# Kernel tuning notes

Hardware: AMD Instinct MI355X
Metric: run time of the kernel (lower is better)

The kernel has to match this reference:

```python
import jax, jax.numpy as jnp
import numpy as np

B, N_OBJ, OBJ_D = 256, 36, 2048
ATT_D, EMB_D, DEC_D, VOCAB, T = 1024, 1024, 1024, 10000, 20


def setup_inputs() -> dict:
    key = jax.random.key(0)
    ks = jax.random.split(key, 16)
    s = lambda *d: 1.0 / np.sqrt(d[-1])
    inp = {
        'encoder_out': jax.random.normal(ks[0], (B, EMB_D), jnp.float32),
        'objects': jax.random.normal(ks[1], (B, N_OBJ, OBJ_D), jnp.float32),
        'encoded_captions': jax.random.randint(ks[2], (B, T), 0, VOCAB),
        'caption_lengths': jax.random.randint(ks[3], (B, 1), 1, T + 1),
        'emb_table': jax.random.normal(ks[4], (VOCAB, EMB_D), jnp.float32) * 0.02,
        'W_enc_att': jax.random.normal(ks[5], (ATT_D, OBJ_D), jnp.float32) * s(OBJ_D),
        'b_enc_att': jnp.zeros((ATT_D,), jnp.float32),
        'W_dec_att': jax.random.normal(ks[6], (ATT_D, DEC_D), jnp.float32) * s(DEC_D),
        'b_dec_att': jnp.zeros((ATT_D,), jnp.float32),
        'w_full_att': jax.random.normal(ks[7], (1, ATT_D), jnp.float32) * s(ATT_D),
        'b_full_att': jnp.zeros((1,), jnp.float32),
        'W_fbeta': jax.random.normal(ks[8], (OBJ_D, DEC_D), jnp.float32) * s(DEC_D),
        'b_fbeta': jnp.zeros((OBJ_D,), jnp.float32),
        'W_ih': jax.random.normal(ks[9], (4 * DEC_D, EMB_D + OBJ_D), jnp.float32) * s(EMB_D + OBJ_D),
        'W_hh': jax.random.normal(ks[10], (4 * DEC_D, DEC_D), jnp.float32) * s(DEC_D),
        'b_ih': jnp.zeros((4 * DEC_D,), jnp.float32),
        'b_hh': jnp.zeros((4 * DEC_D,), jnp.float32),
        'W_fc': jax.random.normal(ks[11], (VOCAB, DEC_D), jnp.float32) * s(DEC_D),
        'b_fc': jnp.zeros((VOCAB,), jnp.float32),
    }
    return inp


def reference(encoder_out, objects, encoded_captions, caption_lengths,
              emb_table, W_enc_att, b_enc_att, W_dec_att, b_dec_att,
              w_full_att, b_full_att, W_fbeta, b_fbeta,
              W_ih, W_hh, b_ih, b_hh, W_fc, b_fc):
    lengths = caption_lengths[:, 0]
    sort_ind = jnp.argsort(-lengths)  # descending
    lengths = lengths[sort_ind]
    encoder_out = encoder_out[sort_ind]
    objects = objects[sort_ind]
    encoded_captions = encoded_captions[sort_ind]

    embeddings = emb_table[encoded_captions]  # (B, T, E)
    # step t input: encoder_out at t=0, embeddings[:, t-1] afterwards
    step_x = jnp.concatenate([encoder_out[:, None, :], embeddings[:, : T - 1, :]], axis=1)  # (B,T,E)

    att1 = jnp.einsum('bno,ao->bna', objects, W_enc_att) + b_enc_att  # (B,N,A), h-independent

    def step(carry, xs):
        h, c = carry
        x_t, t = xs  # (B,E), scalar
        active = (t < lengths)[:, None]  # (B,1) -- batch_size_t masking (lengths sorted desc)
        att2 = h @ W_dec_att.T + b_dec_att  # (B,A)
        e = (jax.nn.relu(att1 + att2[:, None, :]) @ w_full_att[0] + b_full_att[0])  # (B,N)
        alpha = jax.nn.softmax(e, axis=1)
        awe = jnp.einsum('bn,bno->bo', alpha, objects)  # (B,O)
        gate = jax.nn.sigmoid(h @ W_fbeta.T + b_fbeta)
        awe = gate * awe
        gates = jnp.concatenate([x_t, awe], axis=-1) @ W_ih.T + b_ih + h @ W_hh.T + b_hh
        i, f, g, o = jnp.split(gates, 4, axis=-1)  # torch LSTMCell order
        c_new = jax.nn.sigmoid(f) * c + jax.nn.sigmoid(i) * jnp.tanh(g)
        h_new = jax.nn.sigmoid(o) * jnp.tanh(c_new)
        h = jnp.where(active, h_new, h)
        c = jnp.where(active, c_new, c)
        preds = h_new @ W_fc.T + b_fc  # dropout in eval mode = identity
        preds = jnp.where(active, preds, 0.0)
        alpha = jnp.where(active, alpha, 0.0)
        return (h, c), (preds, alpha)

    h0 = jnp.zeros((B, DEC_D), objects.dtype)
    c0 = jnp.zeros((B, DEC_D), objects.dtype)
    xs = (jnp.swapaxes(step_x, 0, 1), jnp.arange(T))
    _, (preds, alphas) = jax.lax.scan(step, (h0, c0), xs)
    predictions = jnp.swapaxes(preds, 0, 1)  # (B,T,V)
    alphas = jnp.swapaxes(alphas, 0, 1)      # (B,T,N)
    return predictions, encoded_captions, lengths, alphas, sort_ind
```

## Files before the change

### kernel.cpp

```cpp
#include <hip/hip_runtime.h>
#include <hip/hip_bf16.h>
#include <cstdint>
#include <cstddef>

#define BB 256
#define TT 20
#define NOBJ 36
#define OBJD 2048
#define ATTD 1024
#define DECD 1024
#define VOCAB 10000
#define NBIG  17168
#define NBIGP 17280
#define NSPLIT 7168

typedef unsigned short u16;
typedef __attribute__((ext_vector_type(8))) short short8v;
typedef __attribute__((ext_vector_type(4))) float float4v;

__device__ inline u16 f2bf(float f) {
    __hip_bfloat16 h = __float2bfloat16(f);
    return *reinterpret_cast<u16*>(&h);
}
__device__ inline float bu(u16 u) {
    union { unsigned int i; float f; } x;
    x.i = ((unsigned int)u) << 16;
    return x.f;
}
__device__ inline float sigf(float x) { return 1.f / (1.f + expf(-x)); }

__device__ inline void gload16(const u16* g, u16* l) {
    __builtin_amdgcn_global_load_lds(
        (const __attribute__((address_space(1))) unsigned int*)g,
        (__attribute__((address_space(3))) unsigned int*)l, 16, 0, 0);
}

__global__ __launch_bounds__(256) void sort_kernel(
    const int* __restrict__ lens, int* __restrict__ sidx, int* __restrict__ slen,
    int* __restrict__ cnt, float* __restrict__ out_len, float* __restrict__ out_sind)
{
    __shared__ int L[BB];
    __shared__ int SL[BB];
    const int i = threadIdx.x;
    const int li = lens[i];
    L[i] = li;
    __syncthreads();
    int r = 0;
    for (int j = 0; j < BB; ++j) {
        const int lj = L[j];
        if (lj > li || (lj == li && j < i)) r++;
    }
    sidx[r] = i;
    slen[r] = li;
    SL[r] = li;
    out_sind[r] = (float)i;
    out_len[r]  = (float)li;
    __syncthreads();
    if (i < TT) {
        int cc = 0;
        for (int b = 0; b < BB; ++b) cc += (SL[b] > i);
        cnt[i] = cc;
    }
}

__global__ __launch_bounds__(256) void meta_kernel(
    const int* __restrict__ caps, const int* __restrict__ sidx,
    float* __restrict__ out_caps)
{
    const int idx = blockIdx.x * 256 + threadIdx.x;
    const int p = idx / TT, t = idx % TT;
    out_caps[idx] = (float)caps[sidx[p] * TT + t];
}

__global__ __launch_bounds__(256) void gather_objs(
    const float* __restrict__ objs, const int* __restrict__ sidx,
    u16* __restrict__ objsb)
{
    const int row = blockIdx.x;
    const int b = row / NOBJ, n = row - b * NOBJ;
    const float* src = objs + ((size_t)sidx[b] * NOBJ + n) * OBJD;
    u16* dst = objsb + (size_t)row * OBJD;
    const int tid = threadIdx.x;
    #pragma unroll
    for (int j = 0; j < 2; ++j) {
        float4 v = ((const float4*)src)[tid + 256 * j];
        ushort4 s;
        s.x = f2bf(v.x); s.y = f2bf(v.y); s.z = f2bf(v.z); s.w = f2bf(v.w);
        ((ushort4*)dst)[tid + 256 * j] = s;
    }
}

__global__ __launch_bounds__(256) void convWbig(
    const float* __restrict__ Wda, const float* __restrict__ bda,
    const float* __restrict__ Wfb, const float* __restrict__ bfb,
    const float* __restrict__ Whh,
    const float* __restrict__ Wfc, const float* __restrict__ bfc,
    u16* __restrict__ Wb, float* __restrict__ bcat)
{
    const int n = blockIdx.x;
    const int tid = threadIdx.x;
    const float* src = nullptr;
    float bb = 0.f;
    if (n < 1024)        { src = Wda + (size_t)n * 1024;            bb = bda[n]; }
    else if (n < 3072)   { src = Wfb + (size_t)(n - 1024) * 1024;   bb = bfb[n - 1024]; }
    else if (n < 7168)   { src = Whh + (size_t)(n - 3072) * 1024;   bb = 0.f; }
    else if (n < NBIG)   { src = Wfc + (size_t)(n - 7168) * 1024;   bb = bfc[n - 7168]; }
    u16* dst = Wb + (size_t)n * 1024;
    ushort4 s;
    if (src) {
        float4 v = ((const float4*)src)[tid];
        s.x = f2bf(v.x); s.y = f2bf(v.y); s.z = f2bf(v.z); s.w = f2bf(v.w);
    } else { s.x = s.y = s.z = s.w = 0; }
    ((ushort4*)dst)[tid] = s;
    if (tid == 0) bcat[n] = bb;
}

__global__ __launch_bounds__(256) void convWih(
    const float* __restrict__ Wih, const float* __restrict__ bih,
    const float* __restrict__ bhh, u16* __restrict__ Wb, float* __restrict__ bsum)
{
    const int n = blockIdx.x;
    const int tid = threadIdx.x;
    const float* src = Wih + (size_t)n * 3072;
    u16* dst = Wb + (size_t)n * 3072;
    #pragma unroll
    for (int j = 0; j < 3; ++j) {
        float4 v = ((const float4*)src)[tid + 256 * j];
        ushort4 s;
        s.x = f2bf(v.x); s.y = f2bf(v.y); s.z = f2bf(v.z); s.w = f2bf(v.w);
        ((ushort4*)dst)[tid + 256 * j] = s;
    }
    if (tid == 0) bsum[n] = bih[n] + bhh[n];
}

__global__ __launch_bounds__(256) void convWea(
    const float* __restrict__ Wea, u16* __restrict__ Wb)
{
    const int n = blockIdx.x;
    const int tid = threadIdx.x;
    const float* src = Wea + (size_t)n * OBJD;
    u16* dst = Wb + (size_t)n * OBJD;
    #pragma unroll
    for (int j = 0; j < 2; ++j) {
        float4 v = ((const float4*)src)[tid + 256 * j];
        ushort4 s;
        s.x = f2bf(v.x); s.y = f2bf(v.y); s.z = f2bf(v.z); s.w = f2bf(v.w);
        ((ushort4*)dst)[tid + 256 * j] = s;
    }
}

__global__ __launch_bounds__(256) void embed_kernel(
    const float* __restrict__ enc, const int* __restrict__ caps,
    const float* __restrict__ emb, const int* __restrict__ sidx,
    u16* __restrict__ Xb)
{
    const int blk = blockIdx.x;
    const int t = blk >> 8;
    const int b = blk & 255;
    const int sb = sidx[b];
    const float* src = (t == 0) ? (enc + (size_t)sb * DECD)
                                : (emb + (size_t)caps[sb * TT + (t - 1)] * DECD);
    const int tid = threadIdx.x;
    float4 v = ((const float4*)src)[tid];
    ushort4 s;
    s.x = f2bf(v.x); s.y = f2bf(v.y); s.z = f2bf(v.z); s.w = f2bf(v.w);
    ((ushort4*)(Xb + (size_t)blk * DECD))[tid] = s;
}

__global__ __launch_bounds__(256) void zero_hc(float* __restrict__ h, float* __restrict__ c)
{
    const int idx = blockIdx.x * 256 + threadIdx.x;
    if (idx < BB * DECD) h[idx] = 0.f;
    else                 c[idx - BB * DECD] = 0.f;
}

__global__ __launch_bounds__(256) void hcat0_kernel(
    const float* __restrict__ bcat, float* __restrict__ Hcat)
{
    const int col4 = blockIdx.x * 256 + threadIdx.x;
    const int m = blockIdx.y;
    ((float4*)(Hcat + (size_t)m * 7168))[col4] = ((const float4*)bcat)[col4];
}

__global__ __launch_bounds__(256) void gemm128(
    const u16* __restrict__ A, int lda,
    const u16* __restrict__ B, int ldb,
    const float* __restrict__ bias,
    float* __restrict__ Cf, u16* __restrict__ Cb, int ldc,
    int Nreal, int kzlen, size_t zCstride,
    int nsplit, float* __restrict__ C2, int ldc2, const int* __restrict__ cntp)
{
    __shared__ u16 As[128 * 32];
    __shared__ u16 Bs[128 * 32];
    const int tid = threadIdx.x;
    const int lane = tid & 63;
    const int w = tid >> 6;
    const int wr = w >> 1, wc = w & 1;
    const int m0 = blockIdx.y * 128;
    const int n0 = blockIdx.x * 128;
    const int kbase = blockIdx.z * kzlen;
    A += kbase;
    B += kbase;
    if (Cf) Cf += (size_t)blockIdx.z * zCstride;

    const int act = cntp ? *cntp : (1 << 30);
    float4v acc[4][4];
    #pragma unroll
    for (int i = 0; i < 4; ++i)
        #pragma unroll
        for (int j = 0; j < 4; ++j) acc[i][j] = (float4v){0.f, 0.f, 0.f, 0.f};

    if (m0 < act) {
        const int r0 = (w * 2 + 0) * 16 + (lane >> 2);
        const int r1 = (w * 2 + 1) * 16 + (lane >> 2);
        const int s0 = (lane & 3) ^ ((r0 >> 1) & 3);
        const int s1 = (lane & 3) ^ ((r1 >> 1) & 3);
        const u16* gA0 = A + (size_t)(m0 + r0) * lda + s0 * 8;
        const u16* gA1 = A + (size_t)(m0 + r1) * lda + s1 * 8;
        const u16* gB0 = B + (size_t)(n0 + r0) * ldb + s0 * 8;
        const u16* gB1 = B + (size_t)(n0 + r1) * ldb + s1 * 8;
        u16* lA0 = &As[(w * 2 + 0) * 16 * 32];
        u16* lA1 = &As[(w * 2 + 1) * 16 * 32];
        u16* lB0 = &Bs[(w * 2 + 0) * 16 * 32];
        u16* lB1 = &Bs[(w * 2 + 1) * 16 * 32];

        int ia[4], ib[4];
        #pragma unroll
        for (int mi = 0; mi < 4; ++mi) {
            const int r = wr * 64 + mi * 16 + (lane & 15);
            ia[mi] = r * 32 + (((lane >> 4) ^ ((r >> 1) & 3)) << 3);
        }
        #pragma unroll
        for (int nj = 0; nj < 4; ++nj) {
            const int r = wc * 64 + nj * 16 + (lane & 15);
            ib[nj] = r * 32 + (((lane >> 4) ^ ((r >> 1) & 3)) << 3);
        }

        const int nk = kzlen >> 5;
        for (int it = 0; it < nk; ++it) {
            gload16(gA0, lA0);
            gload16(gA1, lA1);
            gload16(gB0, lB0);
            gload16(gB1, lB1);
            gA0 += 32; gA1 += 32; gB0 += 32; gB1 += 32;
            __syncthreads();
            short8v av[4], bv[4];
            #pragma unroll
            for (int mi = 0; mi < 4; ++mi) av[mi] = *(const short8v*)&As[ia[mi]];
            #pragma unroll
            for (int nj = 0; nj < 4; ++nj) bv[nj] = *(const short8v*)&Bs[ib[nj]];
            #pragma unroll
            for (int mi = 0; mi < 4; ++mi)
                #pragma unroll
                for (int nj = 0; nj < 4; ++nj)
                    acc[mi][nj] = __builtin_amdgcn_mfma_f32_16x16x32_bf16(
                        av[mi], bv[nj], acc[mi][nj], 0, 0, 0);
            __syncthreads();
        }
    }

    #pragma unroll
    for (int mi = 0; mi < 4; ++mi) {
        const int mbase = m0 + wr * 64 + mi * 16 + ((lane >> 4) << 2);
        #pragma unroll
        for (int nj = 0; nj < 4; ++nj) {
            const int n = n0 + wc * 64 + nj * 16 + (lane & 15);
            if (n >= Nreal) continue;
            const float bval = bias ? bias[n] : 0.f;
            #pragma unroll
            for (int r = 0; r < 4; ++r) {
                const int m = mbase + r;
                const float v = acc[mi][nj][r] + bval;
                if (n < nsplit) {
                    if (Cb) Cb[(size_t)m * ldc + n] = f2bf(v);
                    else    Cf[(size_t)m * ldc + n] = v;
                } else {
                    C2[(size_t)m * ldc2 + (n - nsplit)] = (m < act) ? v : 0.f;
                }
            }
        }
    }
}

__global__ __launch_bounds__(256) void attn_kernel(
    const u16* __restrict__ att1b, const float* __restrict__ Hcat,
    const u16* __restrict__ objsb,
    const float* __restrict__ wfa, const float* __restrict__ bfa,
    const int* __restrict__ slen, int t,
    float* __restrict__ out_alph, u16* __restrict__ aweb)
{
    const int b = blockIdx.x, z = blockIdx.y, tid = threadIdx.x;
    const bool active = t < slen[b];
    if (!active) {
        if (z == 0 && tid < NOBJ)
            out_alph[((size_t)b * TT + t) * NOBJ + tid] = 0.f;
        return;
    }
    __shared__ float wred[4][40];
    __shared__ float es[40];
    __shared__ float alph[40];
    const int lane = tid & 63, w = tid >> 6;
    const float* hrow = Hcat + (size_t)b * 7168;
    const float4 h4 = ((const float4*)hrow)[tid];
    const float4 w4 = ((const float4*)wfa)[tid];
    const u16* a1base = att1b + (size_t)b * NOBJ * ATTD;

    float ep[NOBJ];
    #pragma unroll
    for (int n = 0; n < NOBJ; ++n) {
        ushort4 a4 = ((const ushort4*)(a1base + (size_t)n * ATTD))[tid];
        const float v0 = fmaxf(bu(a4.x) + h4.x, 0.f);
        const float v1 = fmaxf(bu(a4.y) + h4.y, 0.f);
        const float v2 = fmaxf(bu(a4.z) + h4.z, 0.f);
        const float v3 = fmaxf(bu(a4.w) + h4.w, 0.f);
        ep[n] = v0 * w4.x + v1 * w4.y + v2 * w4.z + v3 * w4.w;
    }
    #pragma unroll
    for (int n = 0; n < NOBJ; ++n) {
        float p = ep[n];
        #pragma unroll
        for (int off = 32; off > 0; off >>= 1) p += __shfl_down(p, off, 64);
        if (lane == 0) wred[w][n] = p;
    }
    __syncthreads();
    if (tid < NOBJ)
        es[tid] = wred[0][tid] + wred[1][tid] + wred[2][tid] + wred[3][tid] + bfa[0];
    __syncthreads();
    if (tid == 0) {
        float m = es[0];
        for (int n = 1; n < NOBJ; ++n) m = fmaxf(m, es[n]);
        float s = 0.f;
        for (int n = 0; n < NOBJ; ++n) { const float e = expf(es[n] - m); alph[n] = e; s += e; }
        const float inv = 1.f / s;
        for (int n = 0; n < NOBJ; ++n) alph[n] *= inv;
    }
    __syncthreads();
    if (z == 0 && tid < NOBJ)
        out_alph[((size_t)b * TT + t) * NOBJ + tid] = alph[tid];

    float acc[4] = {0.f, 0.f, 0.f, 0.f};
    const u16* ob = objsb + (size_t)b * NOBJ * OBJD + z * 1024 + tid * 4;
    #pragma unroll 4
    for (int n = 0; n < NOBJ; ++n) {
        const ushort4 ov = *(const ushort4*)(ob + (size_t)n * OBJD);
        const float al = alph[n];
        acc[0] = fmaf(al, bu(ov.x), acc[0]);
        acc[1] = fmaf(al, bu(ov.y), acc[1]);
        acc[2] = fmaf(al, bu(ov.z), acc[2]);
        acc[3] = fmaf(al, bu(ov.w), acc[3]);
    }
    const float4 g0 = *(const float4*)(hrow + 1024 + z * 1024 + tid * 4);
    ushort4 st;
    st.x = f2bf(acc[0] * sigf(g0.x));
    st.y = f2bf(acc[1] * sigf(g0.y));
    st.z = f2bf(acc[2] * sigf(g0.z));
    st.w = f2bf(acc[3] * sigf(g0.w));
    *(ushort4*)&aweb[(size_t)b * 2048 + z * 1024 + tid * 4] = st;
}

__global__ __launch_bounds__(256) void lstm_kernel(
    const float* __restrict__ G2p, const u16* __restrict__ Gxb,
    const float* __restrict__ Hcat,
    float* __restrict__ h, float* __restrict__ c, u16* __restrict__ hb,
    const int* __restrict__ slen, int t)
{
    const int idx = blockIdx.x * 256 + threadIdx.x;
    const int b = idx >> 8, d4 = idx & 255;
    if (t >= slen[b]) return;
    const float4* pw = (const float4*)(Hcat + (size_t)b * 7168 + 3072);
    const u16* gx = Gxb + ((size_t)(t * BB + b)) * 4096;

    float4 g[4];
    #pragma unroll
    for (int q = 0; q < 4; ++q) {
        const ushort4 xv = ((const ushort4*)(gx + q * 1024))[d4];
        float4 s;
        s.x = bu(xv.x); s.y = bu(xv.y); s.z = bu(xv.z); s.w = bu(xv.w);
        const float4 hv = pw[q * 256 + d4];
        s.x += hv.x; s.y += hv.y; s.z += hv.z; s.w += hv.w;
        #pragma unroll
        for (int p = 0; p < 4; ++p) {
            const float4 pv = ((const float4*)G2p)[(size_t)p * (BB * 1024) + b * 1024 + q * 256 + d4];
            s.x += pv.x; s.y += pv.y; s.z += pv.z; s.w += pv.w;
        }
        g[q] = s;
    }
    float4* hp = (float4*)(h + (size_t)b * 1024);
    float4* cp = (float4*)(c + (size_t)b * 1024);
    const float4 cold = cp[d4];
    float4 cn, hn;
    {
        const float si = sigf(g[0].x), sf = sigf(g[1].x), so = sigf(g[3].x);
        cn.x = sf * cold.x + si * tanhf(g[2].x); hn.x = so * tanhf(cn.x);
    }
    {
        const float si = sigf(g[0].y), sf = sigf(g[1].y), so = sigf(g[3].y);
        cn.y = sf * cold.y + si * tanhf(g[2].y); hn.y = so * tanhf(cn.y);
    }
    {
        const float si = sigf(g[0].z), sf = sigf(g[1].z), so = sigf(g[3].z);
        cn.z = sf * cold.z + si * tanhf(g[2].z); hn.z = so * tanhf(cn.z);
    }
    {
        const float si = sigf(g[0].w), sf = sigf(g[1].w), so = sigf(g[3].w);
        cn.w = sf * cold.w + si * tanhf(g[2].w); hn.w = so * tanhf(cn.w);
    }
    hp[d4] = hn;
    cp[d4] = cn;
    ushort4 s;
    s.x = f2bf(hn.x); s.y = f2bf(hn.y); s.z = f2bf(hn.z); s.w = f2bf(hn.w);
    ((ushort4*)(hb + (size_t)b * 1024))[d4] = s;
}

extern "C" void kernel_launch(void* const* d_in, const int* in_sizes, int n_in,
                              void* d_out, int out_size, void* d_ws, size_t ws_size,
                              hipStream_t stream)
{
    const float* enc  = (const float*)d_in[0];
    const float* objs = (const float*)d_in[1];
    const int*   caps = (const int*)d_in[2];
    const int*   clen = (const int*)d_in[3];
    const float* emb  = (const float*)d_in[4];
    const float* Wea  = (const float*)d_in[5];
    const float* bea  = (const float*)d_in[6];
    const float* Wda  = (const float*)d_in[7];
    const float* bda  = (const float*)d_in[8];
    const float* wfa  = (const float*)d_in[9];
    const float* bfa  = (const float*)d_in[10];
    const float* Wfb  = (const float*)d_in[11];
    const float* bfb  = (const float*)d_in[12];
    const float* Wih  = (const float*)d_in[13];
    const float* Whh  = (const float*)d_in[14];
    const float* bih  = (const float*)d_in[15];
    const float* bhh  = (const float*)d_in[16];
    const float* Wfc  = (const float*)d_in[17];
    const float* bfc  = (const float*)d_in[18];

    float* outP     = (float*)d_out;
    float* out_caps = outP + (size_t)BB * TT * VOCAB;
    float* out_len  = out_caps + BB * TT;
    float* out_alph = out_len + BB;
    float* out_sind = out_alph + (size_t)BB * TT * NOBJ;

    char* wp = (char*)d_ws;
    auto alloc = [&](size_t bytes) -> void* {
        void* r = (void*)wp;
        wp += (bytes + 255) & ~(size_t)255;
        return r;
    };
    int*   sidx  = (int*)alloc(BB * 4);
    int*   slen  = (int*)alloc(BB * 4);
    int*   cnt   = (int*)alloc(32 * 4);
    u16*   objsb = (u16*)alloc((size_t)BB * NOBJ * OBJD * 2);
    u16*   Wbigb = (u16*)alloc((size_t)NBIGP * 1024 * 2);
    float* bcat  = (float*)alloc(NBIGP * 4);
    u16*   Wihb  = (u16*)alloc((size_t)4096 * 3072 * 2);
    float* bsum  = (float*)alloc(4096 * 4);
    u16*   Weab  = (u16*)alloc((size_t)1024 * OBJD * 2);
    u16*   att1b = (u16*)alloc((size_t)BB * NOBJ * ATTD * 2);
    u16*   Xb    = (u16*)alloc((size_t)TT * BB * DECD * 2);
    u16*   Gxb   = (u16*)alloc((size_t)TT * BB * 4096 * 2);
    float* Hcat  = (float*)alloc((size_t)BB * 7168 * 4);
    u16*   aweb  = (u16*)alloc((size_t)BB * 2048 * 2);
    float* G2p   = (float*)alloc((size_t)4 * BB * 4096 * 4);
    float* h     = (float*)alloc((size_t)BB * DECD * 4);
    float* c     = (float*)alloc((size_t)BB * DECD * 4);
    u16*   hb    = (u16*)alloc((size_t)BB * DECD * 2);
    (void)ws_size; (void)in_sizes; (void)n_in; (void)out_size;

    sort_kernel<<<1, 256, 0, stream>>>(clen, sidx, slen, cnt, out_len, out_sind);
    meta_kernel<<<20, 256, 0, stream>>>(caps, sidx, out_caps);
    gather_objs<<<BB * NOBJ, 256, 0, stream>>>(objs, sidx, objsb);
    convWbig<<<NBIGP, 256, 0, stream>>>(Wda, bda, Wfb, bfb, Whh, Wfc, bfc, Wbigb, bcat);
    convWih<<<4096, 256, 0, stream>>>(Wih, bih, bhh, Wihb, bsum);
    convWea<<<1024, 256, 0, stream>>>(Wea, Weab);
    embed_kernel<<<TT * BB, 256, 0, stream>>>(enc, caps, emb, sidx, Xb);
    zero_hc<<<2048, 256, 0, stream>>>(h, c);
    hcat0_kernel<<<dim3(7, 256), 256, 0, stream>>>(bcat, Hcat);

    gemm128<<<dim3(8, 72, 1), 256, 0, stream>>>(
        objsb, OBJD, Weab, OBJD, bea, nullptr, att1b, ATTD,
        ATTD, OBJD, 0, 1 << 30, nullptr, 0, nullptr);

    gemm128<<<dim3(32, 40, 1), 256, 0, stream>>>(
        Xb, DECD, Wihb, 3072, bsum, nullptr, Gxb, 4096,
        4096, DECD, 0, 1 << 30, nullptr, 0, nullptr);

    for (int t = 0; t < TT; ++t) {
        attn_kernel<<<dim3(BB, 2), 256, 0, stream>>>(
            att1b, Hcat, objsb, wfa, bfa, slen, t, out_alph, aweb);
        gemm128<<<dim3(32, 2, 4), 256, 0, stream>>>(
            aweb, 2048, Wihb + 1024, 3072, nullptr, G2p, nullptr, 4096,
            4096, 512, (size_t)BB * 4096, 1 << 30, nullptr, 0, cnt + t);
        lstm_kernel<<<256, 256, 0, stream>>>(G2p, Gxb, Hcat, h, c, hb, slen, t);
        gemm128<<<dim3(NBIGP / 128, 2, 1), 256, 0, stream>>>(
            hb, DECD, Wbigb, DECD, bcat, Hcat, nullptr, 7168,
            NBIG, DECD, 0, NSPLIT, outP + (size_t)t * VOCAB, TT * VOCAB, cnt + t);
    }
}
```

Baseline: 1.872 ms.

## Triple-buffer GEMM shared-memory loads, pair M tiles per N block, parallelize softmax

The GEMM main loop moves from a single shared buffer with two barriers per k-step to a three-stage ring. Global loads are issued three tiles ahead, with explicit vmcnt waits and raised wave priority around the MFMAs, so memory latency overlaps with compute. For the per-step GEMMs, the grid is remapped so the two M tiles sharing a weight N tile are adjacent block indices, which should improve L2 reuse of the weights. The attention softmax now uses wave shuffle reductions instead of a single-thread serial loop. Shared memory per block triples, which may lower occupancy.

Result: faster. 1.704 ms (-9.0%).

```diff
diff --git a/kernel.cpp b/kernel.cpp
--- a/kernel.cpp
+++ b/kernel.cpp
@@ -187,17 +187,20 @@
     const u16* __restrict__ B, int ldb,
     const float* __restrict__ bias,
     float* __restrict__ Cf, u16* __restrict__ Cb, int ldc,
-    int Nreal, int kzlen, size_t zCstride,
+    int Nreal, int kzlen, size_t zCstride, int pairM,
     int nsplit, float* __restrict__ C2, int ldc2, const int* __restrict__ cntp)
 {
-    __shared__ u16 As[128 * 32];
-    __shared__ u16 Bs[128 * 32];
+    __shared__ u16 As[3][128 * 32];
+    __shared__ u16 Bs[3][128 * 32];
     const int tid = threadIdx.x;
     const int lane = tid & 63;
     const int w = tid >> 6;
     const int wr = w >> 1, wc = w & 1;
-    const int m0 = blockIdx.y * 128;
-    const int n0 = blockIdx.x * 128;
+    int nIdx, mIdx;
+    if (pairM) { nIdx = blockIdx.x >> 1; mIdx = blockIdx.x & 1; }
+    else       { nIdx = blockIdx.x;      mIdx = blockIdx.y; }
+    const int m0 = mIdx * 128;
+    const int n0 = nIdx * 128;
     const int kbase = blockIdx.z * kzlen;
     A += kbase;
     B += kbase;
@@ -219,10 +222,8 @@
         const u16* gA1 = A + (size_t)(m0 + r1) * lda + s1 * 8;
         const u16* gB0 = B + (size_t)(n0 + r0) * ldb + s0 * 8;
         const u16* gB1 = B + (size_t)(n0 + r1) * ldb + s1 * 8;
-        u16* lA0 = &As[(w * 2 + 0) * 16 * 32];
-        u16* lA1 = &As[(w * 2 + 1) * 16 * 32];
-        u16* lB0 = &Bs[(w * 2 + 0) * 16 * 32];
-        u16* lB1 = &Bs[(w * 2 + 1) * 16 * 32];
+        const int la0 = (w * 2 + 0) * 16 * 32;
+        const int la1 = (w * 2 + 1) * 16 * 32;
 
         int ia[4], ib[4];
         #pragma unroll
@@ -237,25 +238,45 @@
         }
 
         const int nk = kzlen >> 5;
+        #pragma unroll
+        for (int p = 0; p < 3; ++p) {
+            if (p < nk) {
+                const int ko = p * 32;
+                gload16(gA0 + ko, &As[p][la0]);
+                gload16(gA1 + ko, &As[p][la1]);
+                gload16(gB0 + ko, &Bs[p][la0]);
+                gload16(gB1 + ko, &Bs[p][la1]);
+            }
+        }
+        int cur = 0;
         for (int it = 0; it < nk; ++it) {
-            gload16(gA0, lA0);
-            gload16(gA1, lA1);
-            gload16(gB0, lB0);
-            gload16(gB1, lB1);
-            gA0 += 32; gA1 += 32; gB0 += 32; gB1 += 32;
-            __syncthreads();
+            const int rem = nk - 1 - it;
+            if (rem >= 2)      asm volatile("s_waitcnt vmcnt(8)" ::: "memory");
+            else if (rem == 1) asm volatile("s_waitcnt vmcnt(4)" ::: "memory");
+            else               asm volatile("s_waitcnt vmcnt(0)" ::: "memory");
+            __builtin_amdgcn_s_barrier();
             short8v av[4], bv[4];
             #pragma unroll
-            for (int mi = 0; mi < 4; ++mi) av[mi] = *(const short8v*)&As[ia[mi]];
+            for (int mi = 0; mi < 4; ++mi) av[mi] = *(const short8v*)&As[cur][ia[mi]];
             #pragma unroll
-            for (int nj = 0; nj < 4; ++nj) bv[nj] = *(const short8v*)&Bs[ib[nj]];
+            for (int nj = 0; nj < 4; ++nj) bv[nj] = *(const short8v*)&Bs[cur][ib[nj]];
+            __builtin_amdgcn_s_setprio(1);
             #pragma unroll
             for (int mi = 0; mi < 4; ++mi)
                 #pragma unroll
                 for (int nj = 0; nj < 4; ++nj)
                     acc[mi][nj] = __builtin_amdgcn_mfma_f32_16x16x32_bf16(
                         av[mi], bv[nj], acc[mi][nj], 0, 0, 0);
-            __syncthreads();
+            __builtin_amdgcn_s_setprio(0);
+            __builtin_amdgcn_s_barrier();
+            if (it + 3 < nk) {
+                const int ko = (it + 3) * 32;
+                gload16(gA0 + ko, &As[cur][la0]);
+                gload16(gA1 + ko, &As[cur][la1]);
+                gload16(gB0 + ko, &Bs[cur][la0]);
+                gload16(gB1 + ko, &Bs[cur][la1]);
+            }
+            cur = (cur == 2) ? 0 : cur + 1;
         }
     }
 
@@ -326,13 +347,15 @@
     if (tid < NOBJ)
         es[tid] = wred[0][tid] + wred[1][tid] + wred[2][tid] + wred[3][tid] + bfa[0];
     __syncthreads();
-    if (tid == 0) {
-        float m = es[0];
-        for (int n = 1; n < NOBJ; ++n) m = fmaxf(m, es[n]);
-        float s = 0.f;
-        for (int n = 0; n < NOBJ; ++n) { const float e = expf(es[n] - m); alph[n] = e; s += e; }
-        const float inv = 1.f / s;
-        for (int n = 0; n < NOBJ; ++n) alph[n] *= inv;
+    if (tid < 64) {
+        float mv = (tid < NOBJ) ? es[tid] : -1e30f;
+        #pragma unroll
+        for (int off = 32; off > 0; off >>= 1) mv = fmaxf(mv, __shfl_xor(mv, off, 64));
+        float e = (tid < NOBJ) ? expf(es[tid] - mv) : 0.f;
+        float s = e;
+        #pragma unroll
+        for (int off = 32; off > 0; off >>= 1) s += __shfl_xor(s, off, 64);
+        if (tid < NOBJ) alph[tid] = e / s;
     }
     __syncthreads();
     if (z == 0 && tid < NOBJ)
@@ -480,21 +503,21 @@
 
     gemm128<<<dim3(8, 72, 1), 256, 0, stream>>>(
         objsb, OBJD, Weab, OBJD, bea, nullptr, att1b, ATTD,
-        ATTD, OBJD, 0, 1 << 30, nullptr, 0, nullptr);
+        ATTD, OBJD, 0, 0, 1 << 30, nullptr, 0, nullptr);
 
     gemm128<<<dim3(32, 40, 1), 256, 0, stream>>>(
         Xb, DECD, Wihb, 3072, bsum, nullptr, Gxb, 4096,
-        4096, DECD, 0, 1 << 30, nullptr, 0, nullptr);
+        4096, DECD, 0, 0, 1 << 30, nullptr, 0, nullptr);
 
     for (int t = 0; t < TT; ++t) {
         attn_kernel<<<dim3(BB, 2), 256, 0, stream>>>(
             att1b, Hcat, objsb, wfa, bfa, slen, t, out_alph, aweb);
-        gemm128<<<dim3(32, 2, 4), 256, 0, stream>>>(
+        gemm128<<<dim3(64, 1, 4), 256, 0, stream>>>(
             aweb, 2048, Wihb + 1024, 3072, nullptr, G2p, nullptr, 4096,
-            4096, 512, (size_t)BB * 4096, 1 << 30, nullptr, 0, cnt + t);
+            4096, 512, (size_t)BB * 4096, 1, 1 << 30, nullptr, 0, cnt + t);
         lstm_kernel<<<256, 256, 0, stream>>>(G2p, Gxb, Hcat, h, c, hb, slen, t);
-        gemm128<<<dim3(NBIGP / 128, 2, 1), 256, 0, stream>>>(
+        gemm128<<<dim3(NBIGP / 64, 1, 1), 256, 0, stream>>>(
             hb, DECD, Wbigb, DECD, bcat, Hcat, nullptr, 7168,
-            NBIG, DECD, 0, NSPLIT, outP + (size_t)t * VOCAB, TT * VOCAB, cnt + t);
-    }
-}
+            NBIG, DECD, 0, 1, NSPLIT, outP + (size_t)t * VOCAB, TT * VOCAB, cnt + t);
+    }
+}
```
